# Kernel tuning notes

Hardware: AMD Instinct MI355X
Metric: run time of the kernel (lower is better)

The kernel has to match this reference:

```python
import jax, jax.numpy as jnp
import numpy as np

HIDDEN = 512
N_CLASSES = 10

def setup_inputs() -> dict:
    key = jax.random.key(0)
    ks = jax.random.split(key, 7)
    B, T, H = 256, 784, HIDDEN
    s_ih = 1.0 / np.sqrt(H)
    inputs = jax.random.normal(ks[0], (B, T), dtype=jnp.float32)
    # nn.LSTMCell(1, H) parameters, gate order i, f, g, o
    W_ih = jax.random.uniform(ks[1], (4 * H, 1), jnp.float32, -s_ih, s_ih)
    W_hh = jax.random.uniform(ks[2], (4 * H, H), jnp.float32, -s_ih, s_ih)
    b_ih = jax.random.uniform(ks[3], (4 * H,), jnp.float32, -s_ih, s_ih)
    b_hh = jax.random.uniform(ks[4], (4 * H,), jnp.float32, -s_ih, s_ih)
    # nn.Linear(H, 10)
    W_lin = jax.random.uniform(ks[5], (N_CLASSES, H), jnp.float32, -s_ih, s_ih)
    b_lin = jax.random.uniform(ks[6], (N_CLASSES,), jnp.float32, -s_ih, s_ih)
    return {"inputs": inputs, "W_ih": W_ih, "W_hh": W_hh, "b_ih": b_ih,
            "b_hh": b_hh, "W_lin": W_lin, "b_lin": b_lin}

def reference(inputs, W_ih, W_hh, b_ih, b_hh, W_lin, b_lin):
    B = inputs.shape[0]
    H = W_hh.shape[1]
    w_in = W_ih[:, 0]          # [4H], input feature dim is 1
    bias = b_ih + b_hh         # [4H]

    def step(carry, x_t):
        h, c = carry
        # gates: [B, 4H] = x contribution + recurrent matmul + bias
        gates = x_t[:, None] * w_in[None, :] + h @ W_hh.T + bias
        i, f, g, o = jnp.split(gates, 4, axis=1)
        c_new = jax.nn.sigmoid(f) * c + jax.nn.sigmoid(i) * jnp.tanh(g)
        h_new = jax.nn.sigmoid(o) * jnp.tanh(c_new)
        return (h_new, c_new), None

    h0 = jnp.zeros((B, H), dtype=inputs.dtype)
    c0 = jnp.zeros((B, H), dtype=inputs.dtype)
    (h_T, _), _ = jax.lax.scan(step, (h0, c0), inputs.T)  # scan over T
    return h_T @ W_lin.T + b_lin  # [B, n_classes]
```

## Files before the change

kernel.cpp:

```cpp
#include <hip/hip_runtime.h>
#include <hip/hip_bf16.h>
#include <cmath>

#define HID 512
#define TSTEPS 784
#define BATCH 256
#define NCLS 10
#define NBLK 256
#define NGRP 16

typedef __bf16 bf16x8 __attribute__((ext_vector_type(8)));
typedef float f32x4 __attribute__((ext_vector_type(4)));
typedef float f32x2 __attribute__((ext_vector_type(2)));
typedef int   i32x4 __attribute__((ext_vector_type(4)));

#define SWS(r) (((unsigned)(r) & 7u) << 4)

#define LDX4_CC(dst, addr) \
    asm volatile("global_load_dwordx4 %0, %1, off sc0 sc1" : "=v"(dst) : "v"(addr) : "memory")
#define STOREDW_CC(addr, val) \
    asm volatile("global_store_dword %0, %1, off sc0 sc1" :: "v"(addr), "v"(val) : "memory")

__device__ __forceinline__ unsigned lddw_cc_wait(const unsigned* a) {
    unsigned d;
    asm volatile("global_load_dword %0, %1, off sc0 sc1\n\ts_waitcnt vmcnt(0)"
                 : "=v"(d) : "v"(a) : "memory");
    return d;
}

__global__ void init_all(const float* __restrict__ x, float* __restrict__ xT,
                         uint4* __restrict__ hz, unsigned* __restrict__ flg) {
    int t = blockIdx.x, tid = threadIdx.x;
    xT[t * BATCH + tid] = x[tid * TSTEPS + t];
    int i = t * 256 + tid;
    if (i < (512 << 10) / 16) hz[i] = make_uint4(0u, 0u, 0u, 0u);
    if (i < NGRP * 64) flg[i] = 0u;
}

__device__ __forceinline__ float sigmoid_f(float v) {
    return __fdividef(1.f, 1.f + __expf(-v));
}
__device__ __forceinline__ float tanh_f(float v) {
    float e = __expf(fminf(fmaxf(2.f * v, -30.f), 30.f));
    return __fdividef(e - 1.f, e + 1.f);
}

__global__ __launch_bounds__(512)
void lstm_persist(const float* __restrict__ xT,
                  const float* __restrict__ W_hh,
                  const float* __restrict__ w_in,
                  const float* __restrict__ b_ih,
                  const float* __restrict__ b_hh,
                  __bf16* __restrict__ h0,
                  __bf16* __restrict__ h1,
                  float* __restrict__ hf,
                  unsigned* __restrict__ flg)
{
    __shared__ __align__(16) __bf16 wlds[128 * HID];
    __shared__ __align__(16) __bf16 hlds[16 * HID];
    __shared__ float gl[4][16][33];
    __shared__ float xl[16];

    const int tid  = threadIdx.x;
    const int lane = tid & 63;
    const int w    = tid >> 6;
    const int s    = w & 3;
    const int ch   = w >> 2;
    const int bg   = blockIdx.x >> 4;
    const int cs   = blockIdx.x & 15;
    const int b0   = bg * 16;
    const int j0   = cs * 32;
    const int rlo  = lane & 15;
    const int khi  = (lane >> 4) * 8;

    unsigned* flags = flg + bg * 64;

    {
        int r = tid >> 2;
        int q = tid & 3;
        int gs = r >> 5, jj = r & 31;
        const float* src = W_hh + (size_t)(gs * HID + j0 + jj) * HID + q * 128;
        char* wp = (char*)wlds;
        unsigned rowb = (unsigned)r * (HID * 2);
        unsigned sw   = SWS(r);
        #pragma unroll
        for (int cc = 0; cc < 128; cc += 8) {
            float4 va = *(const float4*)(src + cc);
            float4 vb = *(const float4*)(src + cc + 4);
            bf16x8 pk;
            pk[0]=(__bf16)va.x; pk[1]=(__bf16)va.y; pk[2]=(__bf16)va.z; pk[3]=(__bf16)va.w;
            pk[4]=(__bf16)vb.x; pk[5]=(__bf16)vb.y; pk[6]=(__bf16)vb.z; pk[7]=(__bf16)vb.w;
            *(bf16x8*)(wp + ((rowb + (unsigned)(q * 128 + cc) * 2) ^ sw)) = pk;
        }
    }

    const int Rc = tid >> 4;
    const int c2 = (tid & 15) * 2;
    float win_r[4][2], bias_r[4][2];
    #pragma unroll
    for (int g = 0; g < 4; ++g)
        #pragma unroll
        for (int ii = 0; ii < 2; ++ii) {
            int idx = g * HID + j0 + c2 + ii;
            win_r[g][ii]  = w_in[idx];
            bias_r[g][ii] = b_ih[idx] + b_hh[idx];
        }
    float creg[2] = {0.f, 0.f};

    const int rS  = tid & 15;
    const int seg = tid >> 4;
    const unsigned rowbS = (unsigned)rS * (HID * 2);
    const unsigned swS   = SWS(rS);
    const unsigned* myflag = flags + (seg >> 1);

    const unsigned rBb = (unsigned)(s * 32 + ch * 16 + rlo) * (HID * 2);
    const unsigned swB = SWS(rlo);
    const char* wbp = (const char*)wlds;
    const char* hbp = (const char*)hlds;
    char* hwp = (char*)hlds;

    __syncthreads();

    for (int t = 0; t < TSTEPS; ++t) {
        const __bf16* hprev = (t & 1) ? h1 : h0;
        __bf16* hnext       = (t & 1) ? h0 : h1;

        if (tid < 16) xl[tid] = xT[t * BATCH + b0 + tid];
        {
            while (lddw_cc_wait(myflag) < (unsigned)t) __builtin_amdgcn_s_sleep(1);
            const __bf16* gsrc = hprev + (size_t)(b0 + rS) * HID + seg * 16;
            i32x4 v0, v1;
            LDX4_CC(v0, gsrc);
            LDX4_CC(v1, gsrc + 8);
            asm volatile("s_waitcnt vmcnt(0)" ::: "memory");
            __builtin_amdgcn_sched_barrier(0);
            unsigned base = rowbS + (unsigned)seg * 32u;
            *(i32x4*)(hwp + ((base +  0u) ^ swS)) = v0;
            *(i32x4*)(hwp + ((base + 16u) ^ swS)) = v1;
        }
        __syncthreads();

        f32x4 acc_e = {0.f,0.f,0.f,0.f}, acc_o = {0.f,0.f,0.f,0.f};
        #pragma unroll
        for (int ks = 0; ks < 16; ks += 2) {
            unsigned colb0 = (unsigned)(khi * 2 + ks * 64);
            unsigned colb1 = colb0 + 64u;
            bf16x8 a0 = *(const bf16x8*)(hbp + (((unsigned)rlo * 1024u + colb0) ^ SWS(rlo)));
            bf16x8 b0f = *(const bf16x8*)(wbp + ((rBb + colb0) ^ swB));
            bf16x8 a1 = *(const bf16x8*)(hbp + (((unsigned)rlo * 1024u + colb1) ^ SWS(rlo)));
            bf16x8 b1f = *(const bf16x8*)(wbp + ((rBb + colb1) ^ swB));
            acc_e = __builtin_amdgcn_mfma_f32_16x16x32_bf16(a0, b0f, acc_e, 0, 0, 0);
            acc_o = __builtin_amdgcn_mfma_f32_16x16x32_bf16(a1, b1f, acc_o, 0, 0, 0);
        }
        f32x4 acc0 = acc_e + acc_o;
        #pragma unroll
        for (int rr = 0; rr < 4; ++rr) {
            int rowl = (lane >> 4) * 4 + rr;
            gl[s][rowl][ch * 16 + rlo] = acc0[rr];
        }
        __syncthreads();

        if (tid < 256) {
            float xv = xl[Rc];
            float hn2[2];
            #pragma unroll
            for (int ii = 0; ii < 2; ++ii) {
                int ccx = c2 + ii;
                float gi = gl[0][Rc][ccx] + xv * win_r[0][ii] + bias_r[0][ii];
                float gf = gl[1][Rc][ccx] + xv * win_r[1][ii] + bias_r[1][ii];
                float gg = gl[2][Rc][ccx] + xv * win_r[2][ii] + bias_r[2][ii];
                float go = gl[3][Rc][ccx] + xv * win_r[3][ii] + bias_r[3][ii];
                float cn = sigmoid_f(gf) * creg[ii] + sigmoid_f(gi) * tanh_f(gg);
                creg[ii] = cn;
                hn2[ii]  = sigmoid_f(go) * tanh_f(cn);
            }
            if (t == TSTEPS - 1) {
                *(f32x2*)(hf + (size_t)(b0 + Rc) * HID + j0 + c2) = (f32x2){hn2[0], hn2[1]};
            } else {
                union { __bf16 b[2]; int i; } u;
                u.b[0] = (__bf16)hn2[0]; u.b[1] = (__bf16)hn2[1];
                __bf16* dst = hnext + (size_t)(b0 + Rc) * HID + j0 + c2;
                STOREDW_CC(dst, u.i);
            }
        }
        if (t == TSTEPS - 1) break;

        asm volatile("s_waitcnt vmcnt(0)" ::: "memory");
        __syncthreads();
        if (tid == 0) STOREDW_CC(flags + cs, (int)(t + 1));
    }
}

__global__ void head(const float* __restrict__ hfp, const float* __restrict__ Wl,
                     const float* __restrict__ bl_, float* __restrict__ out)
{
    __shared__ float hr[HID];
    int b = blockIdx.x;
    for (int k = threadIdx.x; k < HID; k += blockDim.x) hr[k] = hfp[b * HID + k];
    __syncthreads();
    int j = threadIdx.x;
    if (j < NCLS) {
        float acc = bl_[j];
        for (int k = 0; k < HID; ++k) acc += hr[k] * Wl[j * HID + k];
        out[b * NCLS + j] = acc;
    }
}

extern "C" void kernel_launch(void* const* d_in, const int* in_sizes, int n_in,
                              void* d_out, int out_size, void* d_ws, size_t ws_size,
                              hipStream_t stream) {
    const float* inputs = (const float*)d_in[0];
    const float* W_ih   = (const float*)d_in[1];
    const float* W_hh   = (const float*)d_in[2];
    const float* b_ih   = (const float*)d_in[3];
    const float* b_hh   = (const float*)d_in[4];
    const float* W_lin  = (const float*)d_in[5];
    const float* b_lin  = (const float*)d_in[6];

    const size_t OFS_H1  = 256u << 10;
    const size_t OFS_HF  = 512u << 10;
    const size_t OFS_XT  = 1024u << 10;
    const size_t OFS_FLG = OFS_XT + (size_t)TSTEPS * BATCH * 4;
    const size_t NEEDED  = OFS_FLG + NGRP * 64 * 4;
    if (ws_size < NEEDED) return;

    char* ws = (char*)d_ws;
    __bf16* h0 = (__bf16*)ws;
    __bf16* h1 = (__bf16*)(ws + OFS_H1);
    float*  hf = (float*)(ws + OFS_HF);
    float*  xT = (float*)(ws + OFS_XT);
    unsigned* flg = (unsigned*)(ws + OFS_FLG);

    init_all<<<TSTEPS, BATCH, 0, stream>>>(inputs, xT, (uint4*)h0, flg);

    lstm_persist<<<NBLK, 512, 0, stream>>>(xT, W_hh, W_ih, b_ih, b_hh,
                                           h0, h1, hf, flg);

    head<<<BATCH, 64, 0, stream>>>(hf, W_lin, b_lin, (float*)d_out);
}
```

Before: 2.784 ms.

## Use per-wave progress flags and fold input/bias term into MFMA accumulator init

Each wave now publishes its own step flag right after storing its slice of h, which removes the end-of-step block barrier and the single-thread flag store. Consumers wait on the specific wave flag covering their rows, and the spin loop drops s_sleep. The x*w_in+bias term is preloaded into the MFMA accumulator, so the gate stage no longer does that arithmetic or holds those registers. The cost is four times as many flags, more polling traffic, and a busy spin with no sleep.

Result: slower. 3.654 ms (+31.3%).

```diff
diff --git a/kernel.cpp b/kernel.cpp
--- a/kernel.cpp
+++ b/kernel.cpp
@@ -94,24 +94,22 @@
         }
     }
 
+    float win_l, bias_l;
+    {
+        int idx = s * HID + j0 + ch * 16 + rlo;
+        win_l  = w_in[idx];
+        bias_l = b_ih[idx] + b_hh[idx];
+    }
+
     const int Rc = tid >> 4;
     const int c2 = (tid & 15) * 2;
-    float win_r[4][2], bias_r[4][2];
-    #pragma unroll
-    for (int g = 0; g < 4; ++g)
-        #pragma unroll
-        for (int ii = 0; ii < 2; ++ii) {
-            int idx = g * HID + j0 + c2 + ii;
-            win_r[g][ii]  = w_in[idx];
-            bias_r[g][ii] = b_ih[idx] + b_hh[idx];
-        }
     float creg[2] = {0.f, 0.f};
 
     const int rS  = tid & 15;
     const int seg = tid >> 4;
     const unsigned rowbS = (unsigned)rS * (HID * 2);
     const unsigned swS   = SWS(rS);
-    const unsigned* myflag = flags + (seg >> 1);
+    const unsigned* myflag = flags + (seg >> 1) * 4 + (rS >> 2);
 
     const unsigned rBb = (unsigned)(s * 32 + ch * 16 + rlo) * (HID * 2);
     const unsigned swB = SWS(rlo);
@@ -127,7 +125,7 @@
 
         if (tid < 16) xl[tid] = xT[t * BATCH + b0 + tid];
         {
-            while (lddw_cc_wait(myflag) < (unsigned)t) __builtin_amdgcn_s_sleep(1);
+            while (lddw_cc_wait(myflag) < (unsigned)t) {}
             const __bf16* gsrc = hprev + (size_t)(b0 + rS) * HID + seg * 16;
             i32x4 v0, v1;
             LDX4_CC(v0, gsrc);
@@ -140,7 +138,10 @@
         }
         __syncthreads();
 
-        f32x4 acc_e = {0.f,0.f,0.f,0.f}, acc_o = {0.f,0.f,0.f,0.f};
+        f32x4 acc_e, acc_o = {0.f,0.f,0.f,0.f};
+        #pragma unroll
+        for (int rr = 0; rr < 4; ++rr)
+            acc_e[rr] = xl[(lane >> 4) * 4 + rr] * win_l + bias_l;
         #pragma unroll
         for (int ks = 0; ks < 16; ks += 2) {
             unsigned colb0 = (unsigned)(khi * 2 + ks * 64);
@@ -161,15 +162,14 @@
         __syncthreads();
 
         if (tid < 256) {
-            float xv = xl[Rc];
             float hn2[2];
             #pragma unroll
             for (int ii = 0; ii < 2; ++ii) {
                 int ccx = c2 + ii;
-                float gi = gl[0][Rc][ccx] + xv * win_r[0][ii] + bias_r[0][ii];
-                float gf = gl[1][Rc][ccx] + xv * win_r[1][ii] + bias_r[1][ii];
-                float gg = gl[2][Rc][ccx] + xv * win_r[2][ii] + bias_r[2][ii];
-                float go = gl[3][Rc][ccx] + xv * win_r[3][ii] + bias_r[3][ii];
+                float gi = gl[0][Rc][ccx];
+                float gf = gl[1][Rc][ccx];
+                float gg = gl[2][Rc][ccx];
+                float go = gl[3][Rc][ccx];
                 float cn = sigmoid_f(gf) * creg[ii] + sigmoid_f(gi) * tanh_f(gg);
                 creg[ii] = cn;
                 hn2[ii]  = sigmoid_f(go) * tanh_f(cn);
@@ -181,13 +181,11 @@
                 u.b[0] = (__bf16)hn2[0]; u.b[1] = (__bf16)hn2[1];
                 __bf16* dst = hnext + (size_t)(b0 + Rc) * HID + j0 + c2;
                 STOREDW_CC(dst, u.i);
+                asm volatile("s_waitcnt vmcnt(0)" ::: "memory");
+                if ((tid & 63) == 0)
+                    STOREDW_CC(flags + cs * 4 + w, (int)(t + 1));
             }
         }
-        if (t == TSTEPS - 1) break;
-
-        asm volatile("s_waitcnt vmcnt(0)" ::: "memory");
-        __syncthreads();
-        if (tid == 0) STOREDW_CC(flags + cs, (int)(t + 1));
     }
 }
 
```
